# Performance work log

Measured on AMD Instinct MI355X. Metric: run time of the kernel, lower is better.

Reference implementation:

```python
import jax, jax.numpy as jnp
import numpy as np

B, T, IN = 4096, 512, 32
H = [64, 64, 128]
OUT = 10


def _lstm_cell(x, h, c, Wih, Whh, bih, bhh):
    # PyTorch LSTMCell gate order: i, f, g, o
    gates = x @ Wih.T + bih + h @ Whh.T + bhh
    i, f, g, o = jnp.split(gates, 4, axis=-1)
    c_new = jax.nn.sigmoid(f) * c + jax.nn.sigmoid(i) * jnp.tanh(g)
    h_new = jax.nn.sigmoid(o) * jnp.tanh(c_new)
    return h_new, c_new


def setup_inputs() -> dict:
    key = jax.random.key(0)
    ks = jax.random.split(key, 16)
    s = 0.05
    inp = {"x": jax.random.normal(ks[0], (B, T, IN), dtype=jnp.float32)}
    sizes = [
        ("Wih0", (4 * H[0], IN)), ("Whh0", (4 * H[0], H[0])), ("bih0", (4 * H[0],)), ("bhh0", (4 * H[0],)),
        ("Wih1", (4 * H[1], H[0])), ("Whh1", (4 * H[1], H[1])), ("bih1", (4 * H[1],)), ("bhh1", (4 * H[1],)),
        ("Wih2", (4 * H[2], H[1])), ("Whh2", (4 * H[2], H[2])), ("bih2", (4 * H[2],)), ("bhh2", (4 * H[2],)),
        ("Wfc", (OUT, H[2])), ("bfc", (OUT,)),
    ]
    for k, (name, shp) in zip(ks[1:], sizes):
        inp[name] = jax.random.normal(k, shp, dtype=jnp.float32) * s
    return inp


def reference(x, Wih0, Whh0, bih0, bhh0, Wih1, Whh1, bih1, bhh1,
              Wih2, Whh2, bih2, bhh2, Wfc, bfc):
    b = x.shape[0]
    h0 = jnp.zeros((b, H[0]), x.dtype)
    c0 = jnp.zeros((b, H[0]), x.dtype)
    h1 = jnp.zeros((b, H[1]), x.dtype)
    c1 = jnp.zeros((b, H[1]), x.dtype)
    h2 = jnp.zeros((b, H[2]), x.dtype)
    c2 = jnp.zeros((b, H[2]), x.dtype)

    def step(carry, xt):
        h0, c0, h1, c1, h2, c2 = carry
        h0, c0 = _lstm_cell(xt, h0, c0, Wih0, Whh0, bih0, bhh0)
        h1, c1 = _lstm_cell(h0, h1, c1, Wih1, Whh1, bih1, bhh1)
        h2, c2 = _lstm_cell(h1, h2, c2, Wih2, Whh2, bih2, bhh2)
        return (h0, c0, h1, c1, h2, c2), None

    xs = jnp.swapaxes(x, 0, 1)  # [T, B, IN]
    (h0, c0, h1, c1, h2, c2), _ = jax.lax.scan(step, (h0, c0, h1, c1, h2, c2), xs)
    return h2 @ Wfc.T + bfc
```

## Files before the change

kernel.cpp:

```cpp
#include <hip/hip_runtime.h>


using f32x4  = __attribute__((ext_vector_type(4))) float;
using bf16x8 = __attribute__((ext_vector_type(8))) __bf16;

#define KS (-1.442695041f)
#define KT (-2.885390082f)

__device__ __forceinline__ float bf2f(__bf16 b) {
  unsigned short s = __builtin_bit_cast(unsigned short, b);
  unsigned u = ((unsigned)s) << 16;
  return __builtin_bit_cast(float, u);
}

__device__ __forceinline__ float lstm_h(float ai, float af, float ag, float ao,
                                        float bi0, float bi1, float bi2, float bi3,
                                        float& cs) {
  float Ei = __builtin_amdgcn_exp2f(fmaf(KS, ai, bi0));
  float Ef = __builtin_amdgcn_exp2f(fmaf(KS, af, bi1));
  float Eg = __builtin_amdgcn_exp2f(fmaf(KT, ag, bi2));
  float Eo = __builtin_amdgcn_exp2f(fmaf(KS, ao, bi3));
  float Pi = 1.0f + Ei, Pf = 1.0f + Ef, Pg = 1.0f + Eg, Po = 1.0f + Eo;
  float PiPg = Pi * Pg;
  float N    = fmaf(Pf, 1.0f - Eg, cs * PiPg);
  float nc   = N * __builtin_amdgcn_rcpf(Pf * PiPg);
  cs = nc;
  float En = __builtin_amdgcn_exp2f(KT * nc);
  return (1.0f - En) * __builtin_amdgcn_rcpf(fmaf(Po, En, Po));
}

#define MF(A, Bv, C) __builtin_amdgcn_mfma_f32_16x16x32_bf16((A), (Bv), (C), 0, 0, 0)
#define PIN_A(v) asm volatile("" : "+a"(v))

__device__ __forceinline__ bf16x8 ldw8(const float* p) {
  float4 v0 = *(const float4*)p;
  float4 v1 = *(const float4*)(p + 4);
  bf16x8 r;
  r[0] = (__bf16)v0.x; r[1] = (__bf16)v0.y; r[2] = (__bf16)v0.z; r[3] = (__bf16)v0.w;
  r[4] = (__bf16)v1.x; r[5] = (__bf16)v1.y; r[6] = (__bf16)v1.z; r[7] = (__bf16)v1.w;
  return r;
}

__global__ __launch_bounds__(512)
void lstm_kernel(const float* __restrict__ x,
                 const float* __restrict__ Wih0, const float* __restrict__ Whh0,
                 const float* __restrict__ bih0, const float* __restrict__ bhh0,
                 const float* __restrict__ Wih1, const float* __restrict__ Whh1,
                 const float* __restrict__ bih1, const float* __restrict__ bhh1,
                 const float* __restrict__ Wih2, const float* __restrict__ Whh2,
                 const float* __restrict__ bih2, const float* __restrict__ bhh2,
                 const float* __restrict__ Wfc, const float* __restrict__ bfc,
                 float* __restrict__ out) {
  __shared__ __align__(16) __bf16 h0s[2][16][72];
  __shared__ __align__(16) __bf16 h1s[2][16][72];
  __shared__ __align__(16) __bf16 h2s[2][16][136];
  __shared__ __align__(16) __bf16 wih2l[512][72];

  const int tid = threadIdx.x;
  const int w   = tid >> 6;
  const bool g01 = (w < 4);
  const int gw  = w & 3;
  const int l   = tid & 63;
  const int l15 = l & 15;
  const int lg  = l >> 4;
  const int k0  = lg * 8;
  const int r0  = blockIdx.x << 4;

  for (int i = tid; i < 2 * 16 * 72; i += 512) {
    (&h0s[0][0][0])[i] = __bf16(0.f);
    (&h1s[0][0][0])[i] = __bf16(0.f);
  }
  for (int i = tid; i < 2 * 16 * 136; i += 512) (&h2s[0][0][0])[i] = __bf16(0.f);
  for (int i = tid; i < 512 * 64; i += 512) {
    int row = i >> 6, col = i & 63;
    wih2l[row][col] = (__bf16)Wih2[i];
  }

  bf16x8 AG[32];
#pragma unroll
  for (int i = 0; i < 32; ++i) AG[i] = bf16x8{};
  f32x4  AC[8];
  float  BI[8];
  float  CS[8];
#pragma unroll
  for (int i = 0; i < 8; ++i) CS[i] = 0.f;

  if (g01) {
#pragma unroll
    for (int gi = 0; gi < 4; ++gi) {
      const int row = 16 * (4 * gi + gw) + l15;
      AG[gi] = ldw8(Wih0 + (size_t)row * 32 + k0);
#pragma unroll
      for (int kb = 0; kb < 2; ++kb) {
        AG[4 + 2 * gi + kb]  = ldw8(Whh0 + (size_t)row * 64 + kb * 32 + k0);
        AG[12 + 2 * gi + kb] = ldw8(Wih1 + (size_t)row * 64 + kb * 32 + k0);
        AG[20 + 2 * gi + kb] = ldw8(Whh1 + (size_t)row * 64 + kb * 32 + k0);
      }
      const float sc = (gi == 2) ? KT : KS;
      const int c01 = 64 * gi + 16 * gw + l15;
      BI[gi]     = sc * (bih0[c01] + bhh0[c01]);
      BI[4 + gi] = sc * (bih1[c01] + bhh1[c01]);
    }
  } else {
#pragma unroll
    for (int s = 0; s < 2; ++s)
#pragma unroll
      for (int gi = 0; gi < 4; ++gi) {
        const int row = 16 * (8 * gi + 2 * gw + s) + l15;
#pragma unroll
        for (int kk = 0; kk < 4; ++kk)
          AG[16 * s + 4 * gi + kk] = ldw8(Whh2 + (size_t)row * 128 + kk * 32 + k0);
        const float sc = (gi == 2) ? KT : KS;
        const int c2 = 128 * gi + 32 * gw + 16 * s + l15;
        BI[4 * s + gi] = sc * (bih2[c2] + bhh2[c2]);
      }
  }
#pragma unroll
  for (int i = 0; i < 32; ++i) PIN_A(AG[i]);

  const float* xrow = x + (size_t)(r0 + l15) * 512 * 32 + k0;
  float4 nx0 = {0.f, 0.f, 0.f, 0.f}, nx1 = {0.f, 0.f, 0.f, 0.f};
  if (g01) { nx0 = *(const float4*)xrow; nx1 = *(const float4*)(xrow + 4); }

  const f32x4 Z0 = {0.f, 0.f, 0.f, 0.f};

  __syncthreads();

#pragma unroll 1
  for (int t = 0; t <= 512; ++t) {
    const int pb = t & 1, rb = pb ^ 1;

    if (g01) {
      if (t < 512) {
        float4 cx0 = nx0, cx1 = nx1;
        const int tn = (t + 1) & 511;
        nx0 = *(const float4*)(xrow + (size_t)tn * 32);
        nx1 = *(const float4*)(xrow + (size_t)tn * 32 + 4);

        bf16x8 ax;
        ax[0] = (__bf16)cx0.x; ax[1] = (__bf16)cx0.y; ax[2] = (__bf16)cx0.z; ax[3] = (__bf16)cx0.w;
        ax[4] = (__bf16)cx1.x; ax[5] = (__bf16)cx1.y; ax[6] = (__bf16)cx1.z; ax[7] = (__bf16)cx1.w;

        bf16x8 a0 = *(const bf16x8*)&h0s[rb][l15][k0];
        bf16x8 a1 = *(const bf16x8*)&h0s[rb][l15][32 + k0];
#pragma unroll
        for (int gi = 0; gi < 4; ++gi) {
          f32x4 a = Z0;
          a = MF(ax, AG[gi], a);
          a = MF(a0, AG[4 + 2 * gi], a);
          a = MF(a1, AG[5 + 2 * gi], a);
          AC[gi] = a;
        }
#pragma unroll
        for (int j = 0; j < 4; ++j) {
          float h = lstm_h(AC[0][j], AC[1][j], AC[2][j], AC[3][j],
                           BI[0], BI[1], BI[2], BI[3], CS[j]);
          h0s[pb][4 * lg + j][16 * gw + l15] = (__bf16)h;
        }
      }
    } else {
      if (t >= 1) {
        bf16x8 b0 = *(const bf16x8*)&h1s[rb][l15][k0];
        bf16x8 b1 = *(const bf16x8*)&h1s[rb][l15][32 + k0];
        bf16x8 d0 = *(const bf16x8*)&h2s[pb][l15][k0];
        bf16x8 d1 = *(const bf16x8*)&h2s[pb][l15][32 + k0];
        bf16x8 d2 = *(const bf16x8*)&h2s[pb][l15][64 + k0];
        bf16x8 d3 = *(const bf16x8*)&h2s[pb][l15][96 + k0];
#pragma unroll
        for (int gi = 0; gi < 4; ++gi) {
          const int tile = 8 * gi + 2 * gw;
          bf16x8 wa0 = *(const bf16x8*)&wih2l[16 * tile + l15][k0];
          bf16x8 wa1 = *(const bf16x8*)&wih2l[16 * tile + l15][32 + k0];
          f32x4 a = Z0;
          a = MF(b0, wa0, a);
          a = MF(b1, wa1, a);
          a = MF(d0, AG[4 * gi + 0], a);
          a = MF(d1, AG[4 * gi + 1], a);
          a = MF(d2, AG[4 * gi + 2], a);
          a = MF(d3, AG[4 * gi + 3], a);
          AC[gi] = a;
        }
#pragma unroll
        for (int j = 0; j < 4; ++j) {
          float h = lstm_h(AC[0][j], AC[1][j], AC[2][j], AC[3][j],
                           BI[0], BI[1], BI[2], BI[3], CS[j]);
          h2s[rb][4 * lg + j][32 * gw + l15] = (__bf16)h;
        }
#pragma unroll
        for (int gi = 0; gi < 4; ++gi) {
          const int tile = 8 * gi + 2 * gw + 1;
          bf16x8 wa0 = *(const bf16x8*)&wih2l[16 * tile + l15][k0];
          bf16x8 wa1 = *(const bf16x8*)&wih2l[16 * tile + l15][32 + k0];
          f32x4 a = Z0;
          a = MF(b0, wa0, a);
          a = MF(b1, wa1, a);
          a = MF(d0, AG[16 + 4 * gi + 0], a);
          a = MF(d1, AG[16 + 4 * gi + 1], a);
          a = MF(d2, AG[16 + 4 * gi + 2], a);
          a = MF(d3, AG[16 + 4 * gi + 3], a);
          AC[4 + gi] = a;
        }
      }
    }
    __syncthreads();

    if (g01) {
      if (t < 512) {
        bf16x8 a0 = *(const bf16x8*)&h0s[pb][l15][k0];
        bf16x8 a1 = *(const bf16x8*)&h0s[pb][l15][32 + k0];
        bf16x8 b0 = *(const bf16x8*)&h1s[rb][l15][k0];
        bf16x8 b1 = *(const bf16x8*)&h1s[rb][l15][32 + k0];
#pragma unroll
        for (int gi = 0; gi < 4; ++gi) {
          f32x4 a = Z0;
          a = MF(a0, AG[12 + 2 * gi], a);
          a = MF(a1, AG[13 + 2 * gi], a);
          a = MF(b0, AG[20 + 2 * gi], a);
          a = MF(b1, AG[21 + 2 * gi], a);
          AC[gi] = a;
        }
#pragma unroll
        for (int j = 0; j < 4; ++j) {
          float h = lstm_h(AC[0][j], AC[1][j], AC[2][j], AC[3][j],
                           BI[4], BI[5], BI[6], BI[7], CS[4 + j]);
          h1s[pb][4 * lg + j][16 * gw + l15] = (__bf16)h;
        }
      }
    } else {
      if (t >= 1) {
#pragma unroll
        for (int j = 0; j < 4; ++j) {
          float h = lstm_h(AC[4 + 0][j], AC[4 + 1][j], AC[4 + 2][j], AC[4 + 3][j],
                           BI[4], BI[5], BI[6], BI[7], CS[4 + j]);
          h2s[rb][4 * lg + j][32 * gw + 16 + l15] = (__bf16)h;
        }
      }
    }
    __syncthreads();
  }

  if (tid < 160) {
    const int r = tid / 10, o = tid - r * 10;
    float sum = bfc[o];
    for (int u = 0; u < 128; ++u) sum += bf2f(h2s[1][r][u]) * Wfc[o * 128 + u];
    out[(size_t)(r0 + r) * 10 + o] = sum;
  }
}

extern "C" void kernel_launch(void* const* d_in, const int* in_sizes, int n_in,
                              void* d_out, int out_size, void* d_ws, size_t ws_size,
                              hipStream_t stream) {
  const float* x    = (const float*)d_in[0];
  const float* Wih0 = (const float*)d_in[1];
  const float* Whh0 = (const float*)d_in[2];
  const float* bih0 = (const float*)d_in[3];
  const float* bhh0 = (const float*)d_in[4];
  const float* Wih1 = (const float*)d_in[5];
  const float* Whh1 = (const float*)d_in[6];
  const float* bih1 = (const float*)d_in[7];
  const float* bhh1 = (const float*)d_in[8];
  const float* Wih2 = (const float*)d_in[9];
  const float* Whh2 = (const float*)d_in[10];
  const float* bih2 = (const float*)d_in[11];
  const float* bhh2 = (const float*)d_in[12];
  const float* Wfc  = (const float*)d_in[13];
  const float* bfc  = (const float*)d_in[14];

  lstm_kernel<<<256, 512, 0, stream>>>(x, Wih0, Whh0, bih0, bhh0,
                                       Wih1, Whh1, bih1, bhh1,
                                       Wih2, Whh2, bih2, bhh2,
                                       Wfc, bfc, (float*)d_out);
}
```

Measured before the change: 909.2 us.

## Skew LSTM layers into a wavefront pipeline with one barrier per step

Restructures the time loop so layer 0, layer 1 and layer 2 run as a skewed wavefront: at step t layer 0 computes timestep t, layer 1 timestep t-1 and layer 2 timestep t-2. Each layer now reads only the previous iteration's double-buffered state, so the second __syncthreads per step and the split into two phases can be removed. The aim is to halve barrier count and let layer-1 and layer-2 work overlap within one phase. The trade-off is one extra loop iteration for pipeline drain and reworked buffer parity that must stay consistent with the final readout from h2s[1].

```diff
diff --git a/kernel.cpp b/kernel.cpp
--- a/kernel.cpp
+++ b/kernel.cpp
@@ -127,45 +127,67 @@
   __syncthreads();
 
 #pragma unroll 1
-  for (int t = 0; t <= 512; ++t) {
+  for (int t = 0; t <= 513; ++t) {
     const int pb = t & 1, rb = pb ^ 1;
 
     if (g01) {
-      if (t < 512) {
-        float4 cx0 = nx0, cx1 = nx1;
-        const int tn = (t + 1) & 511;
-        nx0 = *(const float4*)(xrow + (size_t)tn * 32);
-        nx1 = *(const float4*)(xrow + (size_t)tn * 32 + 4);
-
-        bf16x8 ax;
-        ax[0] = (__bf16)cx0.x; ax[1] = (__bf16)cx0.y; ax[2] = (__bf16)cx0.z; ax[3] = (__bf16)cx0.w;
-        ax[4] = (__bf16)cx1.x; ax[5] = (__bf16)cx1.y; ax[6] = (__bf16)cx1.z; ax[7] = (__bf16)cx1.w;
-
+      if (t <= 512) {
         bf16x8 a0 = *(const bf16x8*)&h0s[rb][l15][k0];
         bf16x8 a1 = *(const bf16x8*)&h0s[rb][l15][32 + k0];
-#pragma unroll
-        for (int gi = 0; gi < 4; ++gi) {
-          f32x4 a = Z0;
-          a = MF(ax, AG[gi], a);
-          a = MF(a0, AG[4 + 2 * gi], a);
-          a = MF(a1, AG[5 + 2 * gi], a);
-          AC[gi] = a;
-        }
-#pragma unroll
-        for (int j = 0; j < 4; ++j) {
-          float h = lstm_h(AC[0][j], AC[1][j], AC[2][j], AC[3][j],
-                           BI[0], BI[1], BI[2], BI[3], CS[j]);
-          h0s[pb][4 * lg + j][16 * gw + l15] = (__bf16)h;
+
+        if (t < 512) {
+          float4 cx0 = nx0, cx1 = nx1;
+          const int tn = (t + 1) & 511;
+          nx0 = *(const float4*)(xrow + (size_t)tn * 32);
+          nx1 = *(const float4*)(xrow + (size_t)tn * 32 + 4);
+
+          bf16x8 ax;
+          ax[0] = (__bf16)cx0.x; ax[1] = (__bf16)cx0.y; ax[2] = (__bf16)cx0.z; ax[3] = (__bf16)cx0.w;
+          ax[4] = (__bf16)cx1.x; ax[5] = (__bf16)cx1.y; ax[6] = (__bf16)cx1.z; ax[7] = (__bf16)cx1.w;
+#pragma unroll
+          for (int gi = 0; gi < 4; ++gi) {
+            f32x4 a = Z0;
+            a = MF(ax, AG[gi], a);
+            a = MF(a0, AG[4 + 2 * gi], a);
+            a = MF(a1, AG[5 + 2 * gi], a);
+            AC[gi] = a;
+          }
+#pragma unroll
+          for (int j = 0; j < 4; ++j) {
+            float h = lstm_h(AC[0][j], AC[1][j], AC[2][j], AC[3][j],
+                             BI[0], BI[1], BI[2], BI[3], CS[j]);
+            h0s[pb][4 * lg + j][16 * gw + l15] = (__bf16)h;
+          }
+        }
+
+        if (t >= 1) {
+          bf16x8 b0 = *(const bf16x8*)&h1s[pb][l15][k0];
+          bf16x8 b1 = *(const bf16x8*)&h1s[pb][l15][32 + k0];
+#pragma unroll
+          for (int gi = 0; gi < 4; ++gi) {
+            f32x4 a = Z0;
+            a = MF(a0, AG[12 + 2 * gi], a);
+            a = MF(a1, AG[13 + 2 * gi], a);
+            a = MF(b0, AG[20 + 2 * gi], a);
+            a = MF(b1, AG[21 + 2 * gi], a);
+            AC[4 + gi] = a;
+          }
+#pragma unroll
+          for (int j = 0; j < 4; ++j) {
+            float h = lstm_h(AC[4][j], AC[5][j], AC[6][j], AC[7][j],
+                             BI[4], BI[5], BI[6], BI[7], CS[4 + j]);
+            h1s[rb][4 * lg + j][16 * gw + l15] = (__bf16)h;
+          }
         }
       }
     } else {
-      if (t >= 1) {
-        bf16x8 b0 = *(const bf16x8*)&h1s[rb][l15][k0];
-        bf16x8 b1 = *(const bf16x8*)&h1s[rb][l15][32 + k0];
-        bf16x8 d0 = *(const bf16x8*)&h2s[pb][l15][k0];
-        bf16x8 d1 = *(const bf16x8*)&h2s[pb][l15][32 + k0];
-        bf16x8 d2 = *(const bf16x8*)&h2s[pb][l15][64 + k0];
-        bf16x8 d3 = *(const bf16x8*)&h2s[pb][l15][96 + k0];
+      if (t >= 2) {
+        bf16x8 b0 = *(const bf16x8*)&h1s[pb][l15][k0];
+        bf16x8 b1 = *(const bf16x8*)&h1s[pb][l15][32 + k0];
+        bf16x8 d0 = *(const bf16x8*)&h2s[rb][l15][k0];
+        bf16x8 d1 = *(const bf16x8*)&h2s[rb][l15][32 + k0];
+        bf16x8 d2 = *(const bf16x8*)&h2s[rb][l15][64 + k0];
+        bf16x8 d3 = *(const bf16x8*)&h2s[rb][l15][96 + k0];
 #pragma unroll
         for (int gi = 0; gi < 4; ++gi) {
           const int tile = 8 * gi + 2 * gw;
@@ -184,7 +206,7 @@
         for (int j = 0; j < 4; ++j) {
           float h = lstm_h(AC[0][j], AC[1][j], AC[2][j], AC[3][j],
                            BI[0], BI[1], BI[2], BI[3], CS[j]);
-          h2s[rb][4 * lg + j][32 * gw + l15] = (__bf16)h;
+          h2s[pb][4 * lg + j][32 * gw + l15] = (__bf16)h;
         }
 #pragma unroll
         for (int gi = 0; gi < 4; ++gi) {
@@ -200,39 +222,11 @@
           a = MF(d3, AG[16 + 4 * gi + 3], a);
           AC[4 + gi] = a;
         }
-      }
-    }
-    __syncthreads();
-
-    if (g01) {
-      if (t < 512) {
-        bf16x8 a0 = *(const bf16x8*)&h0s[pb][l15][k0];
-        bf16x8 a1 = *(const bf16x8*)&h0s[pb][l15][32 + k0];
-        bf16x8 b0 = *(const bf16x8*)&h1s[rb][l15][k0];
-        bf16x8 b1 = *(const bf16x8*)&h1s[rb][l15][32 + k0];
-#pragma unroll
-        for (int gi = 0; gi < 4; ++gi) {
-          f32x4 a = Z0;
-          a = MF(a0, AG[12 + 2 * gi], a);
-          a = MF(a1, AG[13 + 2 * gi], a);
-          a = MF(b0, AG[20 + 2 * gi], a);
-          a = MF(b1, AG[21 + 2 * gi], a);
-          AC[gi] = a;
-        }
 #pragma unroll
         for (int j = 0; j < 4; ++j) {
-          float h = lstm_h(AC[0][j], AC[1][j], AC[2][j], AC[3][j],
+          float h = lstm_h(AC[4][j], AC[5][j], AC[6][j], AC[7][j],
                            BI[4], BI[5], BI[6], BI[7], CS[4 + j]);
-          h1s[pb][4 * lg + j][16 * gw + l15] = (__bf16)h;
-        }
-      }
-    } else {
-      if (t >= 1) {
-#pragma unroll
-        for (int j = 0; j < 4; ++j) {
-          float h = lstm_h(AC[4 + 0][j], AC[4 + 1][j], AC[4 + 2][j], AC[4 + 3][j],
-                           BI[4], BI[5], BI[6], BI[7], CS[4 + j]);
-          h2s[rb][4 * lg + j][32 * gw + 16 + l15] = (__bf16)h;
+          h2s[pb][4 * lg + j][32 * gw + 16 + l15] = (__bf16)h;
         }
       }
     }
```

Measured after the change: 852.8 us (median of 2 runs). 1.07x faster.
